# Kernel optimization log

Measured on AMD Instinct MI355X. Metric: run time of the kernel, lower is better.

## Reference

```python
import jax, jax.numpy as jnp
import numpy as np

N = 50000      # nodes
E = 800000     # edges
G = 256        # graphs in batch
D_IN = 128     # input_dim
H = 128        # node_hidden_dim
FC = 128       # fc_hidden_dim
OUT = 2        # out_dim
EPS = 1e-5


def _lin_init(key, fan_in, fan_out, bias=True):
    kw, kb = jax.random.split(key)
    w = jax.random.normal(kw, (fan_in, fan_out), jnp.float32) / np.sqrt(fan_in)
    if bias:
        b = jax.random.normal(kb, (fan_out,), jnp.float32) * 0.01
        return w, b
    return w


def setup_inputs() -> dict:
    key = jax.random.key(0)
    ks = jax.random.split(key, 16)
    x = jax.random.normal(ks[0], (N, D_IN), jnp.float32)
    edge_index = jax.random.randint(ks[1], (2, E), 0, N, jnp.int32)
    batch = jnp.sort(jax.random.randint(ks[2], (N,), 0, G, jnp.int32))
    edge_attr = jax.random.uniform(ks[3], (E, 1), jnp.float32)
    # GraphConv params: lin_rel (with bias) + lin_root (no bias)
    w_rel1, b_rel1 = _lin_init(ks[4], D_IN, H)
    w_root1 = _lin_init(ks[5], D_IN, H, bias=False)
    w_rel2, b_rel2 = _lin_init(ks[6], H, 2 * H)
    w_root2 = _lin_init(ks[7], H, 2 * H, bias=False)
    w_rel3, b_rel3 = _lin_init(ks[8], 2 * H, 3 * H)
    w_root3 = _lin_init(ks[9], 2 * H, 3 * H, bias=False)
    # BatchNorm affine params
    gamma1 = jnp.ones((H,), jnp.float32);      beta1 = jnp.zeros((H,), jnp.float32)
    gamma2 = jnp.ones((2 * H,), jnp.float32);  beta2 = jnp.zeros((2 * H,), jnp.float32)
    gamma3 = jnp.ones((3 * H,), jnp.float32);  beta3 = jnp.zeros((3 * H,), jnp.float32)
    # FC head: lin1 in = 3H+6H+9H = 18H
    w_lin1, b_lin1 = _lin_init(ks[10], 18 * H, FC)
    w_lin2, b_lin2 = _lin_init(ks[11], FC, OUT)
    w_lin3, b_lin3 = _lin_init(ks[12], OUT, OUT)
    return dict(x=x, edge_index=edge_index, batch=batch, edge_attr=edge_attr,
                w_rel1=w_rel1, b_rel1=b_rel1, w_root1=w_root1,
                w_rel2=w_rel2, b_rel2=b_rel2, w_root2=w_root2,
                w_rel3=w_rel3, b_rel3=b_rel3, w_root3=w_root3,
                gamma1=gamma1, beta1=beta1, gamma2=gamma2, beta2=beta2,
                gamma3=gamma3, beta3=beta3,
                w_lin1=w_lin1, b_lin1=b_lin1, w_lin2=w_lin2, b_lin2=b_lin2,
                w_lin3=w_lin3, b_lin3=b_lin3)


def _bn(h, gamma, beta):
    # training-mode BatchNorm1d over node axis
    mu = h.mean(0)
    var = h.var(0)
    return (h - mu) * jax.lax.rsqrt(var + EPS) * gamma + beta


def _gconv(h, src, dst, ew, w_rel, b_rel, w_root):
    # PyG GraphConv: lin_rel(sum_j ew_ij * x_j) + lin_root(x_i)
    agg = jax.ops.segment_sum(h[src] * ew[:, None], dst, num_segments=N)
    return agg @ w_rel + b_rel + h @ w_root


def _pool3(h, batch):
    # concat of global max / mean / add pooling per graph
    s = jax.ops.segment_sum(h, batch, num_segments=G)
    cnt = jax.ops.segment_sum(jnp.ones((h.shape[0], 1), h.dtype), batch, num_segments=G)
    mean = s / jnp.maximum(cnt, 1.0)
    m = jax.ops.segment_max(h, batch, num_segments=G)
    m = jnp.where(cnt > 0, m, 0.0)  # guard empty segments
    return jnp.concatenate([m, mean, s], axis=1)


def reference(x, edge_index, batch, edge_attr,
              w_rel1, b_rel1, w_root1, w_rel2, b_rel2, w_root2,
              w_rel3, b_rel3, w_root3,
              gamma1, beta1, gamma2, beta2, gamma3, beta3,
              w_lin1, b_lin1, w_lin2, b_lin2, w_lin3, b_lin3):
    ew = jnp.transpose(edge_attr, (1, 0))[0]            # [E]
    src, dst = edge_index[0], edge_index[1]
    h = _bn(jax.nn.leaky_relu(_gconv(x, src, dst, ew, w_rel1, b_rel1, w_root1)), gamma1, beta1)
    x1 = _pool3(h, batch)
    h = _bn(jax.nn.leaky_relu(_gconv(h, src, dst, ew, w_rel2, b_rel2, w_root2)), gamma2, beta2)
    x2 = _pool3(h, batch)
    h = _bn(jax.nn.leaky_relu(_gconv(h, src, dst, ew, w_rel3, b_rel3, w_root3)), gamma3, beta3)
    x3 = _pool3(h, batch)
    z = jnp.concatenate([x1, x2, x3], axis=1)           # [G, 18H]
    z = jax.nn.relu(z @ w_lin1 + b_lin1)                # dropout is identity in eval
    z = jax.nn.relu(z @ w_lin2 + b_lin2)
    return jax.nn.log_softmax(z @ w_lin3 + b_lin3, axis=-1)
```

## Files before the change

### kernel.cpp

```cpp
#include <hip/hip_runtime.h>
#include <cstdint>
#include <cstddef>

#define N_NODES 50000
#define M_PAD   50048
#define MB_TILES 391
#define N_EDGES 800000
#define N_GRAPH 256
#define Z_DIM   2304
#define NREP    16
#define POOL_TOT (N_GRAPH * (128 + 256 + 384))

static constexpr float LEAKY  = 0.01f;
static constexpr float BN_EPS = 1e-5f;

typedef short short8 __attribute__((ext_vector_type(8)));
typedef float floatx4 __attribute__((ext_vector_type(4)));
typedef const __attribute__((address_space(1))) unsigned int* gas_ptr;
typedef __attribute__((address_space(3))) unsigned int* las_ptr;
typedef unsigned long long ull;

__device__ __forceinline__ unsigned short f2b(float f) {
  union { float f; unsigned int u; } v; v.f = f;
  unsigned int u = v.u;
  unsigned int r = (u + 0x7FFFu + ((u >> 16) & 1u)) >> 16;
  return (unsigned short)r;
}
__device__ __forceinline__ float b2f(unsigned short h) {
  union { unsigned int u; float f; } v; v.u = ((unsigned int)h) << 16;
  return v.f;
}
__device__ __forceinline__ unsigned fkey(float x) {
  unsigned k = __float_as_uint(x);
  return k ^ ((k & 0x80000000u) ? 0xFFFFFFFFu : 0x80000000u);
}
__device__ __forceinline__ float kdec(unsigned k) {
  k ^= (k & 0x80000000u) ? 0x80000000u : 0xFFFFFFFFu;
  return __uint_as_float(k);
}


__global__ void init_all_kernel(int* __restrict__ cntR, int* __restrict__ gcnt,
                                float* __restrict__ sums_all,
                                unsigned* __restrict__ pmaxk, unsigned* __restrict__ pmink,
                                float* __restrict__ psumg) {
  const int i = blockIdx.x * blockDim.x + threadIdx.x;
  if (i < NREP * N_NODES) cntR[i] = 0;
  if (i < N_GRAPH) gcnt[i] = 0;
  if (i < 2 * (128 + 256 + 384)) sums_all[i] = 0.f;
  if (i < POOL_TOT) { pmaxk[i] = 0u; pmink[i] = 0xFFFFFFFFu; psumg[i] = 0.f; }
}


__global__ void hist_rep_kernel(const int* __restrict__ idx, int* __restrict__ cntR, int n) {
  int i = blockIdx.x * blockDim.x + threadIdx.x;
  if (i < n) {
    const int rep = blockIdx.x & (NREP - 1);
    atomicAdd(&cntR[rep * N_NODES + idx[i]], 1);
  }
}

__global__ __launch_bounds__(256) void scan1_fused_kernel(int* __restrict__ cntR,
                                                          int* __restrict__ out,
                                                          int* __restrict__ part, int n) {
  __shared__ int sm[256];
  const int t = threadIdx.x;
  const int base = blockIdx.x * 1024 + t * 4;
  int v[4] = {0, 0, 0, 0};
#pragma unroll
  for (int j = 0; j < 4; ++j) {
    const int d = base + j;
    if (d < n) {
      int s = 0;
#pragma unroll
      for (int r = 0; r < NREP; ++r) {
        const int c = cntR[r * N_NODES + d];
        cntR[r * N_NODES + d] = s;
        s += c;
      }
      v[j] = s;
    }
  }
  const int tsum = v[0] + v[1] + v[2] + v[3];
  sm[t] = tsum;
  __syncthreads();
  for (int off = 1; off < 256; off <<= 1) {
    int x = (t >= off) ? sm[t - off] : 0;
    __syncthreads();
    sm[t] += x;
    __syncthreads();
  }
  const int excl = sm[t] - tsum;
  if (base     < n) out[base]     = excl;
  if (base + 1 < n) out[base + 1] = excl + v[0];
  if (base + 2 < n) out[base + 2] = excl + v[0] + v[1];
  if (base + 3 < n) out[base + 3] = excl + v[0] + v[1] + v[2];
  if (t == 255) part[blockIdx.x] = sm[255];
}

__global__ __launch_bounds__(256) void scan2_kernel(int* __restrict__ part, int nb,
                                                    int* __restrict__ total_out) {
  __shared__ int sm[256];
  const int t = threadIdx.x;
  const int v = (t < nb) ? part[t] : 0;
  sm[t] = v;
  __syncthreads();
  for (int off = 1; off < 256; off <<= 1) {
    int x = (t >= off) ? sm[t - off] : 0;
    __syncthreads();
    sm[t] += x;
    __syncthreads();
  }
  if (t < nb) part[t] = sm[t] - v;
  if (t == 255) *total_out = sm[255];
}

__global__ void scan3_cursor_kernel(int* __restrict__ out, const int* __restrict__ part,
                                    int* __restrict__ cntR, int n) {
  int i = blockIdx.x * blockDim.x + threadIdx.x;
  if (i >= n) return;
  const int rp = out[i] + part[i >> 10];
  out[i] = rp;
#pragma unroll
  for (int r = 0; r < NREP; ++r) cntR[r * N_NODES + i] += rp;
}

__global__ void bucket_kernel(const int* __restrict__ src, const int* __restrict__ dst,
                              const float* __restrict__ ew, int* __restrict__ cntR,
                              ull* __restrict__ epack, int E) {
  int e = blockIdx.x * blockDim.x + threadIdx.x;
  if (e < E) {
    const int rep = blockIdx.x & (NREP - 1);
    const int d = dst[e];
    const int p = atomicAdd(&cntR[rep * N_NODES + d], 1);
    epack[p] = ((ull)__float_as_uint(ew[e]) << 32) | (unsigned)src[e];
  }
}

__global__ __launch_bounds__(256) void hist_batch_kernel(const int* __restrict__ idx,
                                                         int* __restrict__ cnt, int n) {
  __shared__ int lh[N_GRAPH];
  lh[threadIdx.x] = 0;
  __syncthreads();
  int i = blockIdx.x * blockDim.x + threadIdx.x;
  if (i < n) atomicAdd(&lh[idx[i]], 1);
  __syncthreads();
  const int v = lh[threadIdx.x];
  if (v) atomicAdd(&cnt[threadIdx.x], v);
}

__global__ __launch_bounds__(256) void scan256_kernel(const int* __restrict__ cnt,
                                                      int* __restrict__ gptr) {
  __shared__ int sm[256];
  const int t = threadIdx.x;
  const int v = cnt[t];
  sm[t] = v;
  __syncthreads();
  for (int off = 1; off < 256; off <<= 1) {
    int x = (t >= off) ? sm[t - off] : 0;
    __syncthreads();
    sm[t] += x;
    __syncthreads();
  }
  gptr[t] = sm[t] - v;
  if (t == 255) gptr[256] = sm[255];
}


__global__ void cast_bf16_kernel(const float* __restrict__ in,
                                 unsigned short* __restrict__ out, int npair) {
  int i = blockIdx.x * blockDim.x + threadIdx.x;
  if (i >= npair) return;
  float2 v = *(const float2*)(in + 2 * (size_t)i);
  ((unsigned int*)out)[i] = (unsigned int)f2b(v.x) | ((unsigned int)f2b(v.y) << 16);
}

__global__ __launch_bounds__(256) void wt_build_kernel(
    const float* __restrict__ wrel, const float* __restrict__ wroot,
    const float* __restrict__ brel, const float* __restrict__ sums_prev,
    const float* __restrict__ gamma_prev, const float* __restrict__ beta_prev,
    unsigned short* __restrict__ wt, float* __restrict__ u, float* __restrict__ v,
    int K, int N) {
  __shared__ float redu[256];
  __shared__ float redv[256];
  const int n = blockIdx.x;
  const int K2 = 2 * K;
  const float inv_n = 1.f / (float)N_NODES;
  float us = 0.f, vs = 0.f;
  for (int k = threadIdx.x; k < K2; k += 256) {
    const int kk = (k < K) ? k : k - K;
    const float w = (k < K) ? wrel[(size_t)kk * N + n] : wroot[(size_t)kk * N + n];
    float sc = 1.f, sh = 0.f;
    if (sums_prev) {
      const float mu  = sums_prev[kk] * inv_n;
      const float var = sums_prev[K + kk] * inv_n - mu * mu;
      sc = rsqrtf(var + BN_EPS) * gamma_prev[kk];
      sh = beta_prev[kk] - mu * sc;
    }
    wt[(size_t)n * K2 + k] = f2b(w * sc);
    if (k < K) us += sh * w; else vs += sh * w;
  }
  redu[threadIdx.x] = us; redv[threadIdx.x] = vs;
  __syncthreads();
  for (int o = 128; o > 0; o >>= 1) {
    if (threadIdx.x < o) {
      redu[threadIdx.x] += redu[threadIdx.x + o];
      redv[threadIdx.x] += redv[threadIdx.x + o];
    }
    __syncthreads();
  }
  if (threadIdx.x == 0) { u[n] = redu[0]; v[n] = brel[n] + redv[0]; }
}


template <int D>
__global__ void agg_bf16_kernel(const unsigned short* __restrict__ h,
                                const int* __restrict__ rowptr,
                                const ull* __restrict__ epack,
                                unsigned short* __restrict__ agg,
                                float* __restrict__ degw_out) {
  int gid  = blockIdx.x * blockDim.x + threadIdx.x;
  int node = gid >> 6;
  int lane = threadIdx.x & 63;
  if (node >= N_NODES) return;
  const int beg = rowptr[node], end = rowptr[node + 1];
  constexpr int NP = D / 128;
  float acc0[NP], acc1[NP];
#pragma unroll
  for (int i = 0; i < NP; ++i) { acc0[i] = 0.f; acc1[i] = 0.f; }
  float wsum = 0.f;

  for (int c0 = beg; c0 < end; c0 += 64) {
    const int cn = min(64, end - c0);
    ull pk = 0;
    if (lane < cn) pk = epack[c0 + lane];
    const int   su = (int)(unsigned)pk;
    const float wf = __uint_as_float((unsigned)(pk >> 32));
    const int ng = (cn + 7) >> 3;
    for (int g = 0; g < ng; ++g) {
      int ss[8]; float wv[8];
#pragma unroll
      for (int j = 0; j < 8; ++j) {
        ss[j] = __shfl(su, g * 8 + j);
        wv[j] = __shfl(wf, g * 8 + j);
      }
      unsigned uu[8][NP];
#pragma unroll
      for (int j = 0; j < 8; ++j) {
        const unsigned int* row = (const unsigned int*)(h + (size_t)ss[j] * D);
#pragma unroll
        for (int i = 0; i < NP; ++i) uu[j][i] = row[lane + 64 * i];
      }
#pragma unroll
      for (int j = 0; j < 8; ++j) {
        wsum += wv[j];
#pragma unroll
        for (int i = 0; i < NP; ++i) {
          acc0[i] += b2f((unsigned short)(uu[j][i] & 0xFFFF)) * wv[j];
          acc1[i] += b2f((unsigned short)(uu[j][i] >> 16)) * wv[j];
        }
      }
    }
  }

  unsigned int* o = (unsigned int*)(agg + (size_t)node * D);
#pragma unroll
  for (int i = 0; i < NP; ++i)
    o[lane + 64 * i] = (unsigned int)f2b(acc0[i]) | ((unsigned int)f2b(acc1[i]) << 16);
  if (degw_out != nullptr && lane == 0) degw_out[node] = wsum;
}


__global__ __launch_bounds__(256) void gemm_mfma_kernel(
    const unsigned short* __restrict__ Aagg, const unsigned short* __restrict__ Ah,
    const unsigned short* __restrict__ Wt,
    const float* __restrict__ u, const float* __restrict__ v,
    const float* __restrict__ degw, const int* __restrict__ batch,
    unsigned short* __restrict__ outH, float* __restrict__ sums,
    unsigned* __restrict__ pmaxk, unsigned* __restrict__ pmink,
    float* __restrict__ psumg,
    int M, int K, int N) {
  __shared__ unsigned short As[3][128 * 32];
  __shared__ unsigned short Bs[3][128 * 32];
  __shared__ float col_s[256];
  __shared__ float dws[128];
  __shared__ int gbs[128];

  const int NT = N >> 7;
  const int id = blockIdx.x;
  const int xcd = id & 7;
  const int q   = id >> 3;
  const int m_tile = (q / NT) * 8 + xcd;
  if (m_tile >= MB_TILES) return;
  const int m0 = m_tile * 128;
  const int n0 = (q % NT) * 128;

  const int t  = threadIdx.x;
  const int lane = t & 63;
  const int w    = t >> 6;
  const int wm   = (w & 1) * 64;
  const int wn   = (w >> 1) * 64;
  const int l16  = lane & 15;
  const int lq   = lane >> 4;
  const int K2   = 2 * K;

  const int lrow  = lane >> 2;
  const int lslot = lane & 3;

  col_s[t] = 0.f;
  if (t < 128) {
    const int m = m0 + t;
    dws[t] = (m < M) ? degw[m] : 0.f;
    gbs[t] = (m < M) ? batch[m] : -1;
  }

  floatx4 acc[4][4];
#pragma unroll
  for (int i = 0; i < 4; ++i)
#pragma unroll
    for (int j = 0; j < 4; ++j) acc[i][j] = (floatx4){0.f, 0.f, 0.f, 0.f};

  auto stage = [&](unsigned short* Ab, unsigned short* Bb, int k0) {
    const unsigned short* Asrc;
    int kbase;
    if (k0 < K) { Asrc = Aagg; kbase = k0; } else { Asrc = Ah; kbase = k0 - K; }
#pragma unroll
    for (int qq = 0; qq < 2; ++qq) {
      const int row = w * 32 + qq * 16 + lrow;
      const int gc  = (lslot ^ ((row >> 1) & 3)) * 8;
      const unsigned short* gA = Asrc + (size_t)(m0 + row) * K + kbase + gc;
      const unsigned short* gB = Wt + (size_t)(n0 + row) * K2 + k0 + gc;
      __builtin_amdgcn_global_load_lds((gas_ptr)gA, (las_ptr)(Ab + (w * 32 + qq * 16) * 32),
                                       16, 0, 0);
      __builtin_amdgcn_global_load_lds((gas_ptr)gB, (las_ptr)(Bb + (w * 32 + qq * 16) * 32),
                                       16, 0, 0);
    }
  };

  auto compute = [&](const unsigned short* Ab, const unsigned short* Bb) {
    short8 af[4], bfr[4];
#pragma unroll
    for (int i = 0; i < 4; ++i) {
      const int r = wm + i * 16 + l16;
      af[i] = *(const short8*)(Ab + r * 32 + (lq ^ ((r >> 1) & 3)) * 8);
    }
#pragma unroll
    for (int j = 0; j < 4; ++j) {
      const int r = wn + j * 16 + l16;
      bfr[j] = *(const short8*)(Bb + r * 32 + (lq ^ ((r >> 1) & 3)) * 8);
    }
    __builtin_amdgcn_s_setprio(1);
#pragma unroll
    for (int i = 0; i < 4; ++i)
#pragma unroll
      for (int j = 0; j < 4; ++j)
        acc[i][j] = __builtin_amdgcn_mfma_f32_16x16x32_bf16(af[i], bfr[j], acc[i][j], 0, 0, 0);
    __builtin_amdgcn_s_setprio(0);
  };

  const int NSTEP = K2 >> 5;

  unsigned short *A0 = &As[0][0], *A1 = &As[1][0], *A2 = &As[2][0];
  unsigned short *B0 = &Bs[0][0], *B1 = &Bs[1][0], *B2 = &Bs[2][0];

  stage(A0, B0, 0);
  stage(A1, B1, 1 << 5);

  for (int s = 0; s < NSTEP - 1; ++s) {
    asm volatile("s_waitcnt vmcnt(4)" ::: "memory");
    __builtin_amdgcn_s_barrier();
    __builtin_amdgcn_sched_barrier(0);
    if (s + 2 < NSTEP) stage(A2, B2, (s + 2) << 5);
    compute(A0, B0);
    unsigned short* tA = A0; A0 = A1; A1 = A2; A2 = tA;
    unsigned short* tB = B0; B0 = B1; B1 = B2; B2 = tB;
  }
  asm volatile("s_waitcnt vmcnt(0)" ::: "memory");
  __builtin_amdgcn_s_barrier();
  __builtin_amdgcn_sched_barrier(0);
  compute(A0, B0);

  float uu[4], vv[4];
#pragma unroll
  for (int j = 0; j < 4; ++j) {
    const int n = n0 + wn + j * 16 + l16;
    uu[j] = u[n]; vv[j] = v[n];
  }

  const bool wout = (outH != nullptr);
  float ts[4]  = {0.f, 0.f, 0.f, 0.f};
  float tss[4] = {0.f, 0.f, 0.f, 0.f};
#pragma unroll
  for (int i = 0; i < 4; ++i) {
    const int lrow2 = wm + i * 16 + lq * 4;
#pragma unroll
    for (int j = 0; j < 4; ++j) {
      const int n = n0 + wn + j * 16 + l16;
#pragma unroll
      for (int r = 0; r < 4; ++r) {
        const int m = m0 + lrow2 + r;
        if (m < M) {
          float val = acc[i][j][r] + vv[j] + dws[lrow2 + r] * uu[j];
          val = val > 0.f ? val : LEAKY * val;
          if (wout) outH[(size_t)m * N + n] = f2b(val);
          ts[j]  += val;
          tss[j] += val * val;
        }
      }
    }
  }
#pragma unroll
  for (int j = 0; j < 4; ++j) {
    float a = ts[j], b = tss[j];
    a += __shfl_xor(a, 16); a += __shfl_xor(a, 32);
    b += __shfl_xor(b, 16); b += __shfl_xor(b, 32);
    if (lq == 0) {
      const int ci = wn + j * 16 + l16;
      atomicAdd(&col_s[ci], a);
      atomicAdd(&col_s[128 + ci], b);
    }
  }

  const int lastr = min(127, M - 1 - m0);
  const int gmin = gbs[0];
  const int gmax = gbs[lastr];
  for (int g = gmin; g <= gmax; ++g) {
#pragma unroll
    for (int j = 0; j < 4; ++j) {
      float mx = -3.4e38f, mn = 3.4e38f, sm = 0.f;
#pragma unroll
      for (int i = 0; i < 4; ++i) {
        const int lrow2 = wm + i * 16 + lq * 4;
#pragma unroll
        for (int r = 0; r < 4; ++r) {
          const int row = lrow2 + r;
          const int m = m0 + row;
          if (m < M && gbs[row] == g) {
            float val = acc[i][j][r] + vv[j] + dws[row] * uu[j];
            val = val > 0.f ? val : LEAKY * val;
            mx = fmaxf(mx, val); mn = fminf(mn, val); sm += val;
          }
        }
      }
      mx = fmaxf(mx, __shfl_xor(mx, 16)); mx = fmaxf(mx, __shfl_xor(mx, 32));
      mn = fminf(mn, __shfl_xor(mn, 16)); mn = fminf(mn, __shfl_xor(mn, 32));
      sm += __shfl_xor(sm, 16); sm += __shfl_xor(sm, 32);
      if (lq == 0 && mx > -3.3e38f) {
        const size_t pi = (size_t)g * N + (n0 + wn + j * 16 + l16);
        atomicMax(&pmaxk[pi], fkey(mx));
        atomicMin(&pmink[pi], fkey(mn));
        atomicAdd(&psumg[pi], sm);
      }
    }
  }

  __syncthreads();
  if (t < 128) {
    atomicAdd(&sums[n0 + t], col_s[t]);
    atomicAdd(&sums[N + n0 + t], col_s[128 + t]);
  }
}


__global__ void pool_finalize_all_kernel(const unsigned* __restrict__ pmaxk,
                                         const unsigned* __restrict__ pmink,
                                         const float* __restrict__ psumg,
                                         const float* __restrict__ sums_all,
                                         const float* __restrict__ gamma1, const float* __restrict__ beta1,
                                         const float* __restrict__ gamma2, const float* __restrict__ beta2,
                                         const float* __restrict__ gamma3, const float* __restrict__ beta3,
                                         const int* __restrict__ gptr,
                                         float* __restrict__ z) {
  int i = blockIdx.x * blockDim.x + threadIdx.x;
  if (i >= POOL_TOT) return;
  int C, zoff, li;
  const float *sums, *gamma, *beta;
  if (i < N_GRAPH * 128) {
    C = 128; zoff = 0; li = i;
    sums = sums_all; gamma = gamma1; beta = beta1;
  } else if (i < N_GRAPH * (128 + 256)) {
    C = 256; zoff = 384; li = i - N_GRAPH * 128;
    sums = sums_all + 2 * 128; gamma = gamma2; beta = beta2;
  } else {
    C = 384; zoff = 1152; li = i - N_GRAPH * (128 + 256);
    sums = sums_all + 2 * (128 + 256); gamma = gamma3; beta = beta3;
  }
  const int g = li / C, c = li % C;
  const int cnt = gptr[g + 1] - gptr[g];
  const float inv_n = 1.f / (float)N_NODES;
  const float mu  = sums[c] * inv_n;
  const float var = sums[C + c] * inv_n - mu * mu;
  const float sc  = rsqrtf(var + BN_EPS) * gamma[c];
  const float sh  = beta[c] - mu * sc;
  const float mx = kdec(pmaxk[i]);
  const float mn = kdec(pmink[i]);
  const float sm = psumg[i];
  const float zmax = (sc >= 0.f ? mx : mn) * sc + sh;
  const float zsum = sm * sc + (float)cnt * sh;
  float* zg = z + (size_t)g * Z_DIM + zoff;
  zg[c]         = (cnt > 0) ? zmax : 0.f;
  zg[C + c]     = zsum / (float)(cnt > 0 ? cnt : 1);
  zg[2 * C + c] = zsum;
}


__global__ __launch_bounds__(1024) void fc_kernel(const float* __restrict__ z,
                                                  const float* __restrict__ w1, const float* __restrict__ b1,
                                                  const float* __restrict__ w2, const float* __restrict__ b2,
                                                  const float* __restrict__ w3, const float* __restrict__ b3,
                                                  float* __restrict__ out) {
  __shared__ float zs[Z_DIM];
  __shared__ float part[8][128];
  __shared__ float h1s[128];
  __shared__ float red[128][2];
  __shared__ float y2[2];
  const int g  = blockIdx.x;
  const int t  = threadIdx.x;
  const int c  = t & 127;
  const int ks = t >> 7;
  for (int i = t; i < Z_DIM; i += 1024) zs[i] = z[(size_t)g * Z_DIM + i];
  __syncthreads();

  constexpr int KCH = Z_DIM / 8;
  const int k0 = ks * KCH;
  float acc = 0.f;
#pragma unroll 4
  for (int k = k0; k < k0 + KCH; ++k) acc += zs[k] * w1[(size_t)k * 128 + c];
  part[ks][c] = acc;
  __syncthreads();

  if (t < 128) {
    float s = b1[t];
#pragma unroll
    for (int i = 0; i < 8; ++i) s += part[i][t];
    h1s[t] = fmaxf(s, 0.f);
  }
  __syncthreads();
  if (t < 128) {
    red[t][0] = h1s[t] * w2[t * 2 + 0];
    red[t][1] = h1s[t] * w2[t * 2 + 1];
  }
  __syncthreads();
  if (t < 2) {
    float s = b2[t];
    for (int k = 0; k < 128; ++k) s += red[k][t];
    y2[t] = fmaxf(s, 0.f);
  }
  __syncthreads();
  if (t == 0) {
    const float z0 = y2[0] * w3[0] + y2[1] * w3[2] + b3[0];
    const float z1 = y2[0] * w3[1] + y2[1] * w3[3] + b3[1];
    const float m  = fmaxf(z0, z1);
    const float lse = m + logf(expf(z0 - m) + expf(z1 - m));
    out[g * 2 + 0] = z0 - lse;
    out[g * 2 + 1] = z1 - lse;
  }
}


extern "C" void kernel_launch(void* const* d_in, const int* in_sizes, int n_in,
                              void* d_out, int out_size, void* d_ws, size_t ws_size,
                              hipStream_t stream) {
  (void)in_sizes; (void)n_in; (void)out_size; (void)ws_size;
  const float* x        = (const float*)d_in[0];
  const int*   eidx     = (const int*)d_in[1];
  const int*   batch    = (const int*)d_in[2];
  const float* eattr    = (const float*)d_in[3];
  const float* w_rel1   = (const float*)d_in[4];
  const float* b_rel1   = (const float*)d_in[5];
  const float* w_root1  = (const float*)d_in[6];
  const float* w_rel2   = (const float*)d_in[7];
  const float* b_rel2   = (const float*)d_in[8];
  const float* w_root2  = (const float*)d_in[9];
  const float* w_rel3   = (const float*)d_in[10];
  const float* b_rel3   = (const float*)d_in[11];
  const float* w_root3  = (const float*)d_in[12];
  const float* gamma1   = (const float*)d_in[13];
  const float* beta1    = (const float*)d_in[14];
  const float* gamma2   = (const float*)d_in[15];
  const float* beta2    = (const float*)d_in[16];
  const float* gamma3   = (const float*)d_in[17];
  const float* beta3    = (const float*)d_in[18];
  const float* w_lin1   = (const float*)d_in[19];
  const float* b_lin1   = (const float*)d_in[20];
  const float* w_lin2   = (const float*)d_in[21];
  const float* b_lin2   = (const float*)d_in[22];
  const float* w_lin3   = (const float*)d_in[23];
  const float* b_lin3   = (const float*)d_in[24];

  const int* src = eidx;
  const int* dst = eidx + N_EDGES;
  float* outp = (float*)d_out;

  char* ws = (char*)d_ws;
  size_t off = 0;
  auto alloc = [&](size_t bytes) -> void* {
    void* p = ws + off;
    off += (bytes + 255) & ~(size_t)255;
    return p;
  };
  int*   rowptr = (int*)alloc((N_NODES + 1) * sizeof(int));
  int*   cntR   = (int*)alloc((size_t)NREP * N_NODES * sizeof(int));
  int*   gptr   = (int*)alloc((N_GRAPH + 1) * sizeof(int));
  int*   gcnt   = (int*)alloc(N_GRAPH * sizeof(int));
  int*   part   = (int*)alloc(256 * sizeof(int));
  ull*   epack  = (ull*)alloc((size_t)N_EDGES * sizeof(ull));
  float* degw   = (float*)alloc(N_NODES * sizeof(float));
  float* sums_all = (float*)alloc(2 * (128 + 256 + 384) * sizeof(float));
  float* zbuf   = (float*)alloc((size_t)N_GRAPH * Z_DIM * sizeof(float));
  unsigned* pmaxk = (unsigned*)alloc((size_t)POOL_TOT * 4);
  unsigned* pmink = (unsigned*)alloc((size_t)POOL_TOT * 4);
  float*    psumg = (float*)alloc((size_t)POOL_TOT * 4);
  unsigned short* xb   = (unsigned short*)alloc((size_t)M_PAD * 128 * 2);
  unsigned short* hp1  = (unsigned short*)alloc((size_t)M_PAD * 128 * 2);
  unsigned short* hp2  = (unsigned short*)alloc((size_t)M_PAD * 256 * 2);
  unsigned short* aggb = (unsigned short*)alloc((size_t)M_PAD * 256 * 2);
  unsigned short* wt1 = (unsigned short*)alloc((size_t)128 * 256 * 2);
  unsigned short* wt2 = (unsigned short*)alloc((size_t)256 * 256 * 2);
  unsigned short* wt3 = (unsigned short*)alloc((size_t)384 * 512 * 2);
  float* u1 = (float*)alloc(128 * sizeof(float));
  float* v1 = (float*)alloc(128 * sizeof(float));
  float* u2 = (float*)alloc(256 * sizeof(float));
  float* v2 = (float*)alloc(256 * sizeof(float));
  float* u3 = (float*)alloc(384 * sizeof(float));
  float* v3 = (float*)alloc(384 * sizeof(float));

  float* sums1 = sums_all;
  float* sums2 = sums_all + 2 * 128;
  float* sums3 = sums_all + 2 * (128 + 256);
  const int PO1 = 0, PO2 = N_GRAPH * 128, PO3 = N_GRAPH * (128 + 256);

  const int EB = (N_EDGES + 255) / 256;
  const int NB = (N_NODES + 255) / 256;
  const int SB = (N_NODES + 1023) / 1024;

  init_all_kernel<<<(NREP * N_NODES + 255) / 256, 256, 0, stream>>>(
      cntR, gcnt, sums_all, pmaxk, pmink, psumg);

  hist_rep_kernel<<<EB, 256, 0, stream>>>(dst, cntR, N_EDGES);
  scan1_fused_kernel<<<SB, 256, 0, stream>>>(cntR, rowptr, part, N_NODES);
  scan2_kernel<<<1, 256, 0, stream>>>(part, SB, rowptr + N_NODES);
  scan3_cursor_kernel<<<NB, 256, 0, stream>>>(rowptr, part, cntR, N_NODES);
  bucket_kernel<<<EB, 256, 0, stream>>>(src, dst, eattr, cntR, epack, N_EDGES);

  hist_batch_kernel<<<NB, 256, 0, stream>>>(batch, gcnt, N_NODES);
  scan256_kernel<<<1, 256, 0, stream>>>(gcnt, gptr);

  cast_bf16_kernel<<<(N_NODES * 128 / 2 + 255) / 256, 256, 0, stream>>>(x, xb, N_NODES * 128 / 2);
  wt_build_kernel<<<128, 256, 0, stream>>>(w_rel1, w_root1, b_rel1, nullptr, nullptr, nullptr,
                                           wt1, u1, v1, 128, 128);

  const int aggBlocks = (N_NODES * 64 + 255) / 256;

  agg_bf16_kernel<128><<<aggBlocks, 256, 0, stream>>>(xb, rowptr, epack, aggb, degw);
  gemm_mfma_kernel<<<392 * 1, 256, 0, stream>>>(aggb, xb, wt1, u1, v1, degw, batch,
                                                hp1, sums1, pmaxk + PO1, pmink + PO1,
                                                psumg + PO1, N_NODES, 128, 128);
  wt_build_kernel<<<256, 256, 0, stream>>>(w_rel2, w_root2, b_rel2, sums1, gamma1, beta1,
                                           wt2, u2, v2, 128, 256);

  agg_bf16_kernel<128><<<aggBlocks, 256, 0, stream>>>(hp1, rowptr, epack, aggb, nullptr);
  gemm_mfma_kernel<<<392 * 2, 256, 0, stream>>>(aggb, hp1, wt2, u2, v2, degw, batch,
                                                hp2, sums2, pmaxk + PO2, pmink + PO2,
                                                psumg + PO2, N_NODES, 128, 256);
  wt_build_kernel<<<384, 256, 0, stream>>>(w_rel3, w_root3, b_rel3, sums2, gamma2, beta2,
                                           wt3, u3, v3, 256, 384);

  agg_bf16_kernel<256><<<aggBlocks, 256, 0, stream>>>(hp2, rowptr, epack, aggb, nullptr);
  gemm_mfma_kernel<<<392 * 3, 256, 0, stream>>>(aggb, hp2, wt3, u3, v3, degw, batch,
                                                (unsigned short*)nullptr, sums3,
                                                pmaxk + PO3, pmink + PO3, psumg + PO3,
                                                N_NODES, 256, 384);

  pool_finalize_all_kernel<<<(POOL_TOT + 255) / 256, 256, 0, stream>>>(
      pmaxk, pmink, psumg, sums_all, gamma1, beta1, gamma2, beta2, gamma3, beta3, gptr, zbuf);
  fc_kernel<<<N_GRAPH, 1024, 0, stream>>>(zbuf, w_lin1, b_lin1, w_lin2, b_lin2, w_lin3, b_lin3,
                                          outp);
}
```

Measured before the change: 534.3 us.

## Stage boundary-graph pooling partials per tile instead of global atomics

In the GEMM epilogue, max/min/sum pool contributions for graphs at a tile's first and last row now go to shared-memory slots. Each tile writes these slots as plain stores to a per-tile partial buffer, and only graphs strictly inside a tile still use global atomics. The finalize kernel merges the per-tile partials by walking the m-tiles each graph spans. The epilogue also keeps the activated values in the accumulator registers so the pooling loop does not recompute them. This is meant to cut contended global atomics at graph boundaries shared by neighbouring tiles, at the cost of extra buffers and more finalize work.

```diff
diff --git a/kernel.cpp b/kernel.cpp
--- a/kernel.cpp
+++ b/kernel.cpp
@@ -10,9 +10,15 @@
 #define Z_DIM   2304
 #define NREP    16
 #define POOL_TOT (N_GRAPH * (128 + 256 + 384))
+#define PP_L1 (MB_TILES * 1 * 2 * 128)
+#define PP_L2 (MB_TILES * 2 * 2 * 128)
+#define PP_L3 (MB_TILES * 3 * 2 * 128)
+#define PP_TOT (PP_L1 + PP_L2 + PP_L3)
 
 static constexpr float LEAKY  = 0.01f;
 static constexpr float BN_EPS = 1e-5f;
+static constexpr float FNEG   = -3.4e38f;
+static constexpr float FPOS   =  3.4e38f;
 
 typedef short short8 __attribute__((ext_vector_type(8)));
 typedef float floatx4 __attribute__((ext_vector_type(4)));
@@ -279,12 +285,16 @@
     unsigned short* __restrict__ outH, float* __restrict__ sums,
     unsigned* __restrict__ pmaxk, unsigned* __restrict__ pmink,
     float* __restrict__ psumg,
+    float* __restrict__ ppmax, float* __restrict__ ppmin, float* __restrict__ ppsum,
     int M, int K, int N) {
   __shared__ unsigned short As[3][128 * 32];
   __shared__ unsigned short Bs[3][128 * 32];
   __shared__ float col_s[256];
   __shared__ float dws[128];
   __shared__ int gbs[128];
+  __shared__ unsigned plmax[2][128];
+  __shared__ unsigned plmin[2][128];
+  __shared__ float    plsum[2][128];
 
   const int NT = N >> 7;
   const int id = blockIdx.x;
@@ -293,7 +303,8 @@
   const int m_tile = (q / NT) * 8 + xcd;
   if (m_tile >= MB_TILES) return;
   const int m0 = m_tile * 128;
-  const int n0 = (q % NT) * 128;
+  const int nt2 = q % NT;
+  const int n0 = nt2 * 128;
 
   const int t  = threadIdx.x;
   const int lane = t & 63;
@@ -312,6 +323,9 @@
     const int m = m0 + t;
     dws[t] = (m < M) ? degw[m] : 0.f;
     gbs[t] = (m < M) ? batch[m] : -1;
+    plmax[0][t] = fkey(FNEG); plmax[1][t] = fkey(FNEG);
+    plmin[0][t] = fkey(FPOS); plmin[1][t] = fkey(FPOS);
+    plsum[0][t] = 0.f;        plsum[1][t] = 0.f;
   }
 
   floatx4 acc[4][4];
@@ -399,9 +413,10 @@
 #pragma unroll
       for (int r = 0; r < 4; ++r) {
         const int m = m0 + lrow2 + r;
+        float val = acc[i][j][r] + vv[j] + dws[lrow2 + r] * uu[j];
+        val = val > 0.f ? val : LEAKY * val;
+        acc[i][j][r] = val;
         if (m < M) {
-          float val = acc[i][j][r] + vv[j] + dws[lrow2 + r] * uu[j];
-          val = val > 0.f ? val : LEAKY * val;
           if (wout) outH[(size_t)m * N + n] = f2b(val);
           ts[j]  += val;
           tss[j] += val * val;
@@ -425,19 +440,18 @@
   const int gmin = gbs[0];
   const int gmax = gbs[lastr];
   for (int g = gmin; g <= gmax; ++g) {
+    const int gslot = (g == gmin) ? 0 : ((g == gmax) ? 1 : -1);
 #pragma unroll
     for (int j = 0; j < 4; ++j) {
-      float mx = -3.4e38f, mn = 3.4e38f, sm = 0.f;
+      float mx = FNEG, mn = FPOS, sm = 0.f;
 #pragma unroll
       for (int i = 0; i < 4; ++i) {
         const int lrow2 = wm + i * 16 + lq * 4;
 #pragma unroll
         for (int r = 0; r < 4; ++r) {
           const int row = lrow2 + r;
-          const int m = m0 + row;
-          if (m < M && gbs[row] == g) {
-            float val = acc[i][j][r] + vv[j] + dws[row] * uu[j];
-            val = val > 0.f ? val : LEAKY * val;
+          if (m0 + row < M && gbs[row] == g) {
+            const float val = acc[i][j][r];
             mx = fmaxf(mx, val); mn = fminf(mn, val); sm += val;
           }
         }
@@ -445,16 +459,30 @@
       mx = fmaxf(mx, __shfl_xor(mx, 16)); mx = fmaxf(mx, __shfl_xor(mx, 32));
       mn = fminf(mn, __shfl_xor(mn, 16)); mn = fminf(mn, __shfl_xor(mn, 32));
       sm += __shfl_xor(sm, 16); sm += __shfl_xor(sm, 32);
-      if (lq == 0 && mx > -3.3e38f) {
-        const size_t pi = (size_t)g * N + (n0 + wn + j * 16 + l16);
-        atomicMax(&pmaxk[pi], fkey(mx));
-        atomicMin(&pmink[pi], fkey(mn));
-        atomicAdd(&psumg[pi], sm);
-      }
-    }
-  }
-
-  __syncthreads();
+      if (lq == 0) {
+        const int col = wn + j * 16 + l16;
+        if (gslot >= 0) {
+          atomicMax(&plmax[gslot][col], fkey(mx));
+          atomicMin(&plmin[gslot][col], fkey(mn));
+          atomicAdd(&plsum[gslot][col], sm);
+        } else if (mx > -3.3e38f) {
+          const size_t pi = (size_t)g * N + (n0 + col);
+          atomicMax(&pmaxk[pi], fkey(mx));
+          atomicMin(&pmink[pi], fkey(mn));
+          atomicAdd(&psumg[pi], sm);
+        }
+      }
+    }
+  }
+
+  __syncthreads();
+  {
+    const int gs = t >> 7, col = t & 127;
+    const size_t sb = ((size_t)(m_tile * NT + nt2) * 2 + gs) * 128 + col;
+    ppmax[sb] = kdec(plmax[gs][col]);
+    ppmin[sb] = kdec(plmin[gs][col]);
+    ppsum[sb] = plsum[gs][col];
+  }
   if (t < 128) {
     atomicAdd(&sums[n0 + t], col_s[t]);
     atomicAdd(&sums[N + n0 + t], col_s[128 + t]);
@@ -465,36 +493,66 @@
 __global__ void pool_finalize_all_kernel(const unsigned* __restrict__ pmaxk,
                                          const unsigned* __restrict__ pmink,
                                          const float* __restrict__ psumg,
+                                         const float* __restrict__ ppmax,
+                                         const float* __restrict__ ppmin,
+                                         const float* __restrict__ ppsum,
                                          const float* __restrict__ sums_all,
                                          const float* __restrict__ gamma1, const float* __restrict__ beta1,
                                          const float* __restrict__ gamma2, const float* __restrict__ beta2,
                                          const float* __restrict__ gamma3, const float* __restrict__ beta3,
                                          const int* __restrict__ gptr,
+                                         const int* __restrict__ batch,
                                          float* __restrict__ z) {
   int i = blockIdx.x * blockDim.x + threadIdx.x;
   if (i >= POOL_TOT) return;
-  int C, zoff, li;
+  int C, zoff, li, NTL;
+  size_t ppo;
   const float *sums, *gamma, *beta;
   if (i < N_GRAPH * 128) {
-    C = 128; zoff = 0; li = i;
+    C = 128; zoff = 0; li = i; NTL = 1; ppo = 0;
     sums = sums_all; gamma = gamma1; beta = beta1;
   } else if (i < N_GRAPH * (128 + 256)) {
-    C = 256; zoff = 384; li = i - N_GRAPH * 128;
+    C = 256; zoff = 384; li = i - N_GRAPH * 128; NTL = 2; ppo = PP_L1;
     sums = sums_all + 2 * 128; gamma = gamma2; beta = beta2;
   } else {
-    C = 384; zoff = 1152; li = i - N_GRAPH * (128 + 256);
+    C = 384; zoff = 1152; li = i - N_GRAPH * (128 + 256); NTL = 3; ppo = PP_L1 + PP_L2;
     sums = sums_all + 2 * (128 + 256); gamma = gamma3; beta = beta3;
   }
   const int g = li / C, c = li % C;
   const int cnt = gptr[g + 1] - gptr[g];
+
+  float mx = FNEG, mn = FPOS, sm = psumg[i];
+  {
+    const unsigned pk = pmaxk[i];
+    if (pk != 0u) mx = kdec(pk);
+    const unsigned nk = pmink[i];
+    if (nk != 0xFFFFFFFFu) mn = kdec(nk);
+  }
+  if (cnt > 0) {
+    const int mt_lo = gptr[g] >> 7;
+    const int mt_hi = (gptr[g + 1] - 1) >> 7;
+    const int nt = c >> 7, cc = c & 127;
+    for (int mt = mt_lo; mt <= mt_hi; ++mt) {
+      const int g0 = batch[mt << 7];
+      int grel = (g == g0) ? 0 : -1;
+      if (grel < 0) {
+        const int lastm = min((mt << 7) + 127, N_NODES - 1);
+        if (g == batch[lastm]) grel = 1;
+      }
+      if (grel >= 0) {
+        const size_t sb = ppo + ((size_t)(mt * NTL + nt) * 2 + grel) * 128 + cc;
+        mx = fmaxf(mx, ppmax[sb]);
+        mn = fminf(mn, ppmin[sb]);
+        sm += ppsum[sb];
+      }
+    }
+  }
+
   const float inv_n = 1.f / (float)N_NODES;
   const float mu  = sums[c] * inv_n;
   const float var = sums[C + c] * inv_n - mu * mu;
   const float sc  = rsqrtf(var + BN_EPS) * gamma[c];
   const float sh  = beta[c] - mu * sc;
-  const float mx = kdec(pmaxk[i]);
-  const float mn = kdec(pmink[i]);
-  const float sm = psumg[i];
   const float zmax = (sc >= 0.f ? mx : mn) * sc + sh;
   const float zsum = sm * sc + (float)cnt * sh;
   float* zg = z + (size_t)g * Z_DIM + zoff;
@@ -611,6 +669,9 @@
   unsigned* pmaxk = (unsigned*)alloc((size_t)POOL_TOT * 4);
   unsigned* pmink = (unsigned*)alloc((size_t)POOL_TOT * 4);
   float*    psumg = (float*)alloc((size_t)POOL_TOT * 4);
+  float* ppmax = (float*)alloc((size_t)PP_TOT * 4);
+  float* ppmin = (float*)alloc((size_t)PP_TOT * 4);
+  float* ppsum = (float*)alloc((size_t)PP_TOT * 4);
   unsigned short* xb   = (unsigned short*)alloc((size_t)M_PAD * 128 * 2);
   unsigned short* hp1  = (unsigned short*)alloc((size_t)M_PAD * 128 * 2);
   unsigned short* hp2  = (unsigned short*)alloc((size_t)M_PAD * 256 * 2);
@@ -655,14 +716,16 @@
   agg_bf16_kernel<128><<<aggBlocks, 256, 0, stream>>>(xb, rowptr, epack, aggb, degw);
   gemm_mfma_kernel<<<392 * 1, 256, 0, stream>>>(aggb, xb, wt1, u1, v1, degw, batch,
                                                 hp1, sums1, pmaxk + PO1, pmink + PO1,
-                                                psumg + PO1, N_NODES, 128, 128);
+                                                psumg + PO1, ppmax, ppmin, ppsum,
+                                                N_NODES, 128, 128);
   wt_build_kernel<<<256, 256, 0, stream>>>(w_rel2, w_root2, b_rel2, sums1, gamma1, beta1,
                                            wt2, u2, v2, 128, 256);
 
   agg_bf16_kernel<128><<<aggBlocks, 256, 0, stream>>>(hp1, rowptr, epack, aggb, nullptr);
   gemm_mfma_kernel<<<392 * 2, 256, 0, stream>>>(aggb, hp1, wt2, u2, v2, degw, batch,
                                                 hp2, sums2, pmaxk + PO2, pmink + PO2,
-                                                psumg + PO2, N_NODES, 128, 256);
+                                                psumg + PO2, ppmax + PP_L1, ppmin + PP_L1,
+                                                ppsum + PP_L1, N_NODES, 128, 256);
   wt_build_kernel<<<384, 256, 0, stream>>>(w_rel3, w_root3, b_rel3, sums2, gamma2, beta2,
                                            wt3, u3, v3, 256, 384);
 
@@ -670,10 +733,12 @@
   gemm_mfma_kernel<<<392 * 3, 256, 0, stream>>>(aggb, hp2, wt3, u3, v3, degw, batch,
                                                 (unsigned short*)nullptr, sums3,
                                                 pmaxk + PO3, pmink + PO3, psumg + PO3,
-                                                N_NODES, 256, 384);
+                                                ppmax + PP_L1 + PP_L2, ppmin + PP_L1 + PP_L2,
+                                                ppsum + PP_L1 + PP_L2, N_NODES, 256, 384);
 
   pool_finalize_all_kernel<<<(POOL_TOT + 255) / 256, 256, 0, stream>>>(
-      pmaxk, pmink, psumg, sums_all, gamma1, beta1, gamma2, beta2, gamma3, beta3, gptr, zbuf);
+      pmaxk, pmink, psumg, ppmax, ppmin, ppsum, sums_all,
+      gamma1, beta1, gamma2, beta2, gamma3, beta3, gptr, batch, zbuf);
   fc_kernel<<<N_GRAPH, 1024, 0, stream>>>(zbuf, w_lin1, b_lin1, w_lin2, b_lin2, w_lin3, b_lin3,
                                           outp);
 }
```

Result: no change. 533.0 us (-0.2%).
